# Kernel tuning notes

Measured on AMD Instinct MI355X. Metric: run time of the kernel, lower is better.

Reference implementation:

```python
import jax, jax.numpy as jnp
import numpy as np
import math

B, T, E, H = 4, 2048, 1024, 16
ALPHA = 32.0


def setup_inputs() -> dict:
    key = jax.random.key(0)
    ks = jax.random.split(key, 6)
    s = 1.0 / math.sqrt(E)
    return {
        "x": jax.random.normal(ks[0], (B, T, E), dtype=jnp.float32),
        "ch_list": 0,
        "Wq": jax.random.normal(ks[1], (E, E), dtype=jnp.float32) * s,
        "bq": jnp.zeros((E,), jnp.float32),
        "Wk": jax.random.normal(ks[2], (E, E), dtype=jnp.float32) * s,
        "bk": jnp.zeros((E,), jnp.float32),
        "Wv": jax.random.normal(ks[3], (E, E), dtype=jnp.float32) * s,
        "bv": jnp.zeros((E,), jnp.float32),
        "Wp": jax.random.normal(ks[4], (E, E), dtype=jnp.float32) * s,
        "bp": jnp.zeros((E,), jnp.float32),
    }


def reference(x, ch_list, Wq, bq, Wk, bk, Wv, bv, Wp, bp):
    Bx, Tx, Ex = x.shape
    hd = Ex // H  # head dim
    # linear projections (weights stored [in, out]); split heads -> [B,H,T,hd]
    def heads(W, b):
        return (x @ W + b).reshape(Bx, Tx, H, hd).transpose(0, 2, 1, 3)
    q, k, v = heads(Wq, bq), heads(Wk, bk), heads(Wv, bv)
    scale = 1.0 / (ALPHA * math.sqrt(hd))
    qk = jnp.einsum("bhqd,bhkd->bhqk", q * scale, k)  # [B,H,T,T]
    # extra max-rescale BEFORE the causal mask (faithful to original order)
    qk = qk - jnp.max(qk, axis=-1, keepdims=True)
    causal = jnp.tril(jnp.ones((Tx, Tx), dtype=bool))  # [T,T]
    qk = jnp.where(causal[None, None], qk, -jnp.inf)
    att = jax.nn.softmax(qk * ALPHA, axis=-1)  # dropout p=0 -> identity
    y = jnp.einsum("bhqk,bhkd->bhqd", att, v)
    y = y.transpose(0, 2, 1, 3).reshape(Bx, Tx, Ex)
    return y @ Wp + bp
```

## Files before the change

### kernel.cpp

```cpp
#include <hip/hip_runtime.h>
#include <cmath>

typedef unsigned short u16;
typedef unsigned int u32;
typedef __bf16 bf16x8 __attribute__((ext_vector_type(8)));
typedef float  floatx4 __attribute__((ext_vector_type(4)));
typedef float  floatx16 __attribute__((ext_vector_type(16)));
typedef unsigned int u32x4 __attribute__((ext_vector_type(4)));

#define T_DIM 2048
#define E_DIM 1024
#define H_DIM 16
#define HD    64
#define M_DIM 8192
#define NE    8388608
#define E2    1048576
#define QSCALE 0.18033688f

__device__ __forceinline__ u16 f2bf(float f) {
    unsigned u = __builtin_bit_cast(unsigned, f);
    return (u16)((u + 0x7FFFu + ((u >> 16) & 1u)) >> 16);
}
__device__ __forceinline__ u32 pack2bf(float f0, float f1) {
    u32 a0 = __builtin_bit_cast(u32, f0) + 0x8000u;
    u32 a1 = __builtin_bit_cast(u32, f1) + 0x8000u;
    return __builtin_amdgcn_perm(a1, a0, 0x07060302u);
}

__device__ __forceinline__ void gl_lds16(const u16* g, const u16* l) {
    __builtin_amdgcn_global_load_lds(
        (const __attribute__((address_space(1))) void*)g,
        (__attribute__((address_space(3))) void*)l,
        16, 0, 0);
}

__device__ __forceinline__ bf16x8 ld_frag(const u16* p) {
    return *(const bf16x8*)p;
}

__global__ void cvt_x_kernel(const float* __restrict__ x, u16* __restrict__ xb) {
    const size_t i = (size_t)blockIdx.x * 256 + threadIdx.x;
    const float4* s = (const float4*)x + i * 2;
    const float4 a = s[0], b = s[1];
    u16 v[8] __attribute__((aligned(16)));
    v[0]=f2bf(a.x); v[1]=f2bf(a.y); v[2]=f2bf(a.z); v[3]=f2bf(a.w);
    v[4]=f2bf(b.x); v[5]=f2bf(b.y); v[6]=f2bf(b.z); v[7]=f2bf(b.w);
    *(uint4*)(xb + i * 8) = *(const uint4*)v;
}

__global__ void transpose_cvt_kernel(const float* __restrict__ w0, const float* __restrict__ w1,
                                     const float* __restrict__ w2, const float* __restrict__ w3,
                                     u16* __restrict__ out) {
    __shared__ u16 tile[64][65];
    const float* W = blockIdx.z == 0 ? w0 : blockIdx.z == 1 ? w1 : blockIdx.z == 2 ? w2 : w3;
    u16* O = out + (size_t)blockIdx.z * E2;
    const int k0 = blockIdx.y * 64, n0 = blockIdx.x * 64;
    const int r = threadIdx.x >> 2, cp = (threadIdx.x & 3) * 16;
    const float4* src = (const float4*)&W[(size_t)(k0 + r) * E_DIM + n0 + cp];
    #pragma unroll
    for (int j4 = 0; j4 < 4; ++j4) {
        const float4 f = src[j4];
        tile[r][cp + j4*4 + 0] = f2bf(f.x);
        tile[r][cp + j4*4 + 1] = f2bf(f.y);
        tile[r][cp + j4*4 + 2] = f2bf(f.z);
        tile[r][cp + j4*4 + 3] = f2bf(f.w);
    }
    __syncthreads();
    u16 vals[16] __attribute__((aligned(16)));
    #pragma unroll
    for (int j = 0; j < 16; ++j) vals[j] = tile[cp + j][r];
    u16* dst = &O[(size_t)(n0 + r) * E_DIM + k0 + cp];
    *(uint4*)dst       = *(const uint4*)vals;
    *(uint4*)(dst + 8) = *(const uint4*)(vals + 8);
}

__global__ void transpose_v_kernel(const u16* __restrict__ v, u16* __restrict__ vt) {
    __shared__ u16 tile[64][72];
    const int bh = blockIdx.y, t0 = blockIdx.x * 64;
    const int r = threadIdx.x >> 2, cp = (threadIdx.x & 3) * 16;
    const u16* src = &v[((size_t)bh * T_DIM + t0 + r) * HD + cp];
    *(uint4*)&tile[r][cp]     = *(const uint4*)src;
    *(uint4*)&tile[r][cp + 8] = *(const uint4*)(src + 8);
    __syncthreads();
    u16 vals[16] __attribute__((aligned(16)));
    #pragma unroll
    for (int j = 0; j < 16; ++j) vals[j] = tile[cp + j][r];
    u16* dst = &vt[((size_t)bh * HD + r) * T_DIM + t0 + cp];
    *(uint4*)dst       = *(const uint4*)vals;
    *(uint4*)(dst + 8) = *(const uint4*)(vals + 8);
}

template<int REMAP>
__global__ __launch_bounds__(256)
void gemm_bf16_kernel(const u16* __restrict__ A, const u16* __restrict__ Bt,
                      const float* __restrict__ bias0, const float* __restrict__ bias1,
                      const float* __restrict__ bias2, void* __restrict__ outp)
{
    __shared__ u16 As[128 * 32];
    __shared__ u16 Bs[128 * 32];
    const int tid = threadIdx.x;
    const int w = tid >> 6, lane = tid & 63, quad = lane >> 4, l15 = lane & 15;
    const int wm = w >> 1, wn = w & 1;
    const int r0 = blockIdx.y * 128, c0 = blockIdx.x * 128;

    floatx4 acc[4][4];
    #pragma unroll
    for (int mi = 0; mi < 4; ++mi)
        #pragma unroll
        for (int ni = 0; ni < 4; ++ni)
            acc[mi][ni] = (floatx4){0.f, 0.f, 0.f, 0.f};

    for (int k0 = 0; k0 < E_DIM; k0 += 32) {
        __syncthreads();
        #pragma unroll
        for (int i = 0; i < 2; ++i) {
            const int L = i * 256 + tid;
            const unsigned off = __builtin_amdgcn_readfirstlane(i * 4096 + w * 1024);
            gl_lds16(&A [(size_t)(r0 + (L >> 2)) * E_DIM + k0 + (L & 3) * 8], (u16*)((char*)As + off));
            gl_lds16(&Bt[(size_t)(c0 + (L >> 2)) * E_DIM + k0 + (L & 3) * 8], (u16*)((char*)Bs + off));
        }
        __syncthreads();
        bf16x8 Af[4], Bf[4];
        #pragma unroll
        for (int mi = 0; mi < 4; ++mi) Af[mi] = ld_frag(&As[(wm*64 + mi*16 + l15) * 32 + quad*8]);
        #pragma unroll
        for (int ni = 0; ni < 4; ++ni) Bf[ni] = ld_frag(&Bs[(wn*64 + ni*16 + l15) * 32 + quad*8]);
        #pragma unroll
        for (int mi = 0; mi < 4; ++mi)
            #pragma unroll
            for (int ni = 0; ni < 4; ++ni)
                acc[mi][ni] = __builtin_amdgcn_mfma_f32_16x16x32_bf16(Af[mi], Bf[ni], acc[mi][ni], 0, 0, 0);
    }

    #pragma unroll
    for (int ni = 0; ni < 4; ++ni) {
        const int col = c0 + wn * 64 + ni * 16 + l15;
        float bv;
        int which = 0, cc = col;
        if (REMAP == 1) {
            which = col >> 10; cc = col & 1023;
            const float* bp_ = which == 0 ? bias0 : which == 1 ? bias1 : bias2;
            bv = bp_[cc];
        } else {
            bv = bias0[col];
        }
        #pragma unroll
        for (int mi = 0; mi < 4; ++mi) {
            #pragma unroll
            for (int r = 0; r < 4; ++r) {
                const int row = r0 + wm * 64 + mi * 16 + quad * 4 + r;
                float val = acc[mi][ni][r] + bv;
                if (REMAP == 1) {
                    if (which == 0) val *= QSCALE;
                    const int h = cc >> 6, d = cc & 63;
                    const int b = row >> 11, t = row & (T_DIM - 1);
                    ((u16*)outp)[(size_t)which * NE +
                                 (((size_t)(b * H_DIM + h) * T_DIM + t) * HD + d)] = f2bf(val);
                } else {
                    ((float*)outp)[(size_t)row * E_DIM + col] = val;
                }
            }
        }
    }
}

__global__ __launch_bounds__(256, 2)
void attn_kernel(const u16* __restrict__ q, const u16* __restrict__ k,
                 const u16* __restrict__ vt, u16* __restrict__ y)
{
    __shared__ u16 Ks[2][128 * 64];
    __shared__ u16 Vs[2][64 * 128];

    const int tid = threadIdx.x;
    const int w = tid >> 6, lane = tid & 63;
    const int hl = lane >> 5, l31 = lane & 31, l7 = lane & 7;
    const int bh = blockIdx.x;
    const int qt = gridDim.y - 1 - blockIdx.y;
    const int q0 = qt * 128;
    const int b = bh >> 4, h = bh & (H_DIM - 1);
    const size_t qkb = (size_t)bh * (T_DIM * HD);
    const size_t vtb = (size_t)bh * (HD * T_DIM);

    const int qrow = q0 + w * 32 + l31;
    bf16x8 Qf[4];
    #pragma unroll
    for (int kc = 0; kc < 4; ++kc)
        Qf[kc] = ld_frag(&q[qkb + (size_t)qrow * HD + kc * 16 + hl * 8]);

    float rsum = 0.f;
    floatx16 O[2];
    #pragma unroll
    for (int i = 0; i < 16; ++i) { O[0][i] = 0.f; O[1][i] = 0.f; }

    auto stage = [&](int jt, int sel) {
        const int j0 = jt * 128;
        #pragma unroll
        for (int i = 0; i < 4; ++i) {
            const int L = i * 256 + tid;
            const unsigned off = __builtin_amdgcn_readfirstlane(i * 4096 + w * 1024);
            {   const int row = L >> 3, ch = (L & 7) ^ (row & 7);
                gl_lds16(&k[qkb + (size_t)(j0 + row) * HD + ch * 8],
                         (u16*)((char*)&Ks[sel][0] + off)); }
            {   const int row = L >> 4, ch = (L & 15) ^ (row & 7);
                gl_lds16(&vt[vtb + (size_t)row * T_DIM + j0 + ch * 8],
                         (u16*)((char*)&Vs[sel][0] + off)); }
        }
    };

    stage(0, 0);
    for (int jt = 0; jt <= qt; ++jt) {
        __syncthreads();
        if (jt < qt) stage(jt + 1, (jt + 1) & 1);
        const u16* const Kb = &Ks[jt & 1][0];
        const u16* const Vb = &Vs[jt & 1][0];

        const bool diag = (jt == qt);
        const int nkg = diag ? (w + 1) : 4;

        #pragma unroll
        for (int kg = 0; kg < 4; ++kg) {
            if (kg < nkg) {
                floatx16 S;
                #pragma unroll
                for (int i = 0; i < 16; ++i) S[i] = 0.f;
                const int krow = kg * 32 + l31;
                #pragma unroll
                for (int kc = 0; kc < 4; ++kc) {
                    const int ch = (kc * 2 + hl) ^ l7;
                    S = __builtin_amdgcn_mfma_f32_32x32x16_bf16(
                            ld_frag(&Kb[krow * 64 + ch * 8]), Qf[kc], S, 0, 0, 0);
                }

                const bool bnd = diag && (kg == w);
                u32 u[8], ru[8];
                #pragma unroll
                for (int i = 0; i < 8; ++i) {
                    const int row0 = (2*i & 3) + 8 * (i >> 1) + 4 * hl;
                    float p0 = __builtin_amdgcn_exp2f(S[2*i]);
                    float p1 = __builtin_amdgcn_exp2f(S[2*i + 1]);
                    if (bnd && (row0     > l31)) p0 = 0.f;
                    if (bnd && (row0 + 1 > l31)) p1 = 0.f;
                    rsum += p0 + p1;
                    u[i] = pack2bf(p0, p1);
                }
                #pragma unroll
                for (int i = 0; i < 8; ++i) ru[i] = __shfl_xor(u[i], 32, 64);
                const u32x4 f0 = hl ? (u32x4){ru[2], ru[3], u[2], u[3]}
                                    : (u32x4){u[0], u[1], ru[0], ru[1]};
                const u32x4 f1 = hl ? (u32x4){ru[6], ru[7], u[6], u[7]}
                                    : (u32x4){u[4], u[5], ru[4], ru[5]};

                #pragma unroll
                for (int c2 = 0; c2 < 2; ++c2) {
                    const bf16x8 Pf = __builtin_bit_cast(bf16x8, c2 ? f1 : f0);
                    const int kc16 = kg * 4 + c2 * 2 + hl;
                    #pragma unroll
                    for (int dh = 0; dh < 2; ++dh) {
                        const int d = dh * 32 + l31;
                        const int ch = kc16 ^ l7;
                        O[dh] = __builtin_amdgcn_mfma_f32_32x32x16_bf16(
                                    Pf, ld_frag(&Vb[d * 128 + ch * 8]), O[dh], 0, 0, 0);
                    }
                }
            }
        }
    }

    rsum += __shfl_xor(rsum, 32, 64);
    const float linv = 1.0f / rsum;
    #pragma unroll
    for (int i = 0; i < 16; ++i) {
        const int qr = (i & 3) + 8 * (i >> 2) + 4 * hl;
        const float lq = __shfl(linv, qr, 32);
        const int t = q0 + w * 32 + qr;
        const size_t base = ((size_t)(b * T_DIM + t)) * E_DIM + h * HD;
        y[base + l31]      = f2bf(O[0][i] * lq);
        y[base + 32 + l31] = f2bf(O[1][i] * lq);
    }
}

extern "C" void kernel_launch(void* const* d_in, const int* in_sizes, int n_in,
                              void* d_out, int out_size, void* d_ws, size_t ws_size,
                              hipStream_t stream)
{
    const float* x  = (const float*)d_in[0];
    const float* Wq = (const float*)d_in[2];
    const float* bq = (const float*)d_in[3];
    const float* Wk = (const float*)d_in[4];
    const float* bk = (const float*)d_in[5];
    const float* Wv = (const float*)d_in[6];
    const float* bv = (const float*)d_in[7];
    const float* Wp = (const float*)d_in[8];
    const float* bp = (const float*)d_in[9];

    u16* xb  = (u16*)d_ws;
    u16* wt  = xb + NE;
    u16* qb  = wt + 4 * (size_t)E2;
    u16* kb  = qb + NE;
    u16* vb  = kb + NE;
    u16* vtb = vb + NE;
    u16* yb  = vtb + NE;

    cvt_x_kernel<<<NE / (256 * 8), 256, 0, stream>>>(x, xb);
    transpose_cvt_kernel<<<dim3(16, 16, 4), 256, 0, stream>>>(Wq, Wk, Wv, Wp, wt);
    gemm_bf16_kernel<1><<<dim3(24, 64), 256, 0, stream>>>(xb, wt, bq, bk, bv, qb);
    transpose_v_kernel<<<dim3(32, 64), 256, 0, stream>>>(vb, vtb);
    attn_kernel<<<dim3(64, 16), 256, 0, stream>>>(qb, kb, vtb, yb);
    gemm_bf16_kernel<0><<<dim3(8, 64), 256, 0, stream>>>(yb, wt + 3 * (size_t)E2, bp, bp, bp, (float*)d_out);
}
```

Measured before the change: 264.1 us.

## Fuse V transpose into QKV GEMM epilogue and swizzle GEMM LDS tiles

The QKV projection GEMM now writes the V output directly in transposed [bh, d, t] layout, packing four consecutive rows into one 8-byte store. This removes the separate transpose_v kernel and its extra read/write pass over V. The GEMM's LDS layout also gets an XOR swizzle on the 8-element k-chunks, applied on both the global-to-LDS load and the fragment reads, to cut bank conflicts. The transposed V stores are strided by T, which may be less coalesced than the old row-major writes.

New measurement: 254.4 us. 1.04x faster.

```diff
diff --git a/kernel.cpp b/kernel.cpp
--- a/kernel.cpp
+++ b/kernel.cpp
@@ -74,27 +74,12 @@
     *(uint4*)(dst + 8) = *(const uint4*)(vals + 8);
 }
 
-__global__ void transpose_v_kernel(const u16* __restrict__ v, u16* __restrict__ vt) {
-    __shared__ u16 tile[64][72];
-    const int bh = blockIdx.y, t0 = blockIdx.x * 64;
-    const int r = threadIdx.x >> 2, cp = (threadIdx.x & 3) * 16;
-    const u16* src = &v[((size_t)bh * T_DIM + t0 + r) * HD + cp];
-    *(uint4*)&tile[r][cp]     = *(const uint4*)src;
-    *(uint4*)&tile[r][cp + 8] = *(const uint4*)(src + 8);
-    __syncthreads();
-    u16 vals[16] __attribute__((aligned(16)));
-    #pragma unroll
-    for (int j = 0; j < 16; ++j) vals[j] = tile[cp + j][r];
-    u16* dst = &vt[((size_t)bh * HD + r) * T_DIM + t0 + cp];
-    *(uint4*)dst       = *(const uint4*)vals;
-    *(uint4*)(dst + 8) = *(const uint4*)(vals + 8);
-}
-
 template<int REMAP>
 __global__ __launch_bounds__(256)
 void gemm_bf16_kernel(const u16* __restrict__ A, const u16* __restrict__ Bt,
                       const float* __restrict__ bias0, const float* __restrict__ bias1,
-                      const float* __restrict__ bias2, void* __restrict__ outp)
+                      const float* __restrict__ bias2, void* __restrict__ outp,
+                      u16* __restrict__ vtp)
 {
     __shared__ u16 As[128 * 32];
     __shared__ u16 Bs[128 * 32];
@@ -110,21 +95,25 @@
         for (int ni = 0; ni < 4; ++ni)
             acc[mi][ni] = (floatx4){0.f, 0.f, 0.f, 0.f};
 
+    const int fsw = (quad ^ ((l15 >> 1) & 3)) * 8;
+
     for (int k0 = 0; k0 < E_DIM; k0 += 32) {
         __syncthreads();
         #pragma unroll
         for (int i = 0; i < 2; ++i) {
             const int L = i * 256 + tid;
+            const int row = L >> 2, s = L & 3;
+            const int c = s ^ ((row >> 1) & 3);
             const unsigned off = __builtin_amdgcn_readfirstlane(i * 4096 + w * 1024);
-            gl_lds16(&A [(size_t)(r0 + (L >> 2)) * E_DIM + k0 + (L & 3) * 8], (u16*)((char*)As + off));
-            gl_lds16(&Bt[(size_t)(c0 + (L >> 2)) * E_DIM + k0 + (L & 3) * 8], (u16*)((char*)Bs + off));
+            gl_lds16(&A [(size_t)(r0 + row) * E_DIM + k0 + c * 8], (u16*)((char*)As + off));
+            gl_lds16(&Bt[(size_t)(c0 + row) * E_DIM + k0 + c * 8], (u16*)((char*)Bs + off));
         }
         __syncthreads();
         bf16x8 Af[4], Bf[4];
         #pragma unroll
-        for (int mi = 0; mi < 4; ++mi) Af[mi] = ld_frag(&As[(wm*64 + mi*16 + l15) * 32 + quad*8]);
-        #pragma unroll
-        for (int ni = 0; ni < 4; ++ni) Bf[ni] = ld_frag(&Bs[(wn*64 + ni*16 + l15) * 32 + quad*8]);
+        for (int mi = 0; mi < 4; ++mi) Af[mi] = ld_frag(&As[(wm*64 + mi*16 + l15) * 32 + fsw]);
+        #pragma unroll
+        for (int ni = 0; ni < 4; ++ni) Bf[ni] = ld_frag(&Bs[(wn*64 + ni*16 + l15) * 32 + fsw]);
         #pragma unroll
         for (int mi = 0; mi < 4; ++mi)
             #pragma unroll
@@ -146,18 +135,28 @@
         }
         #pragma unroll
         for (int mi = 0; mi < 4; ++mi) {
-            #pragma unroll
-            for (int r = 0; r < 4; ++r) {
-                const int row = r0 + wm * 64 + mi * 16 + quad * 4 + r;
-                float val = acc[mi][ni][r] + bv;
-                if (REMAP == 1) {
-                    if (which == 0) val *= QSCALE;
-                    const int h = cc >> 6, d = cc & 63;
-                    const int b = row >> 11, t = row & (T_DIM - 1);
-                    ((u16*)outp)[(size_t)which * NE +
-                                 (((size_t)(b * H_DIM + h) * T_DIM + t) * HD + d)] = f2bf(val);
-                } else {
-                    ((float*)outp)[(size_t)row * E_DIM + col] = val;
+            if (REMAP == 1 && which == 2) {
+                const int h = cc >> 6, d = cc & 63;
+                const int row0 = r0 + wm * 64 + mi * 16 + quad * 4;
+                const int b = row0 >> 11, t0 = row0 & (T_DIM - 1);
+                uint2 pk;
+                pk.x = pack2bf(acc[mi][ni][0] + bv, acc[mi][ni][1] + bv);
+                pk.y = pack2bf(acc[mi][ni][2] + bv, acc[mi][ni][3] + bv);
+                *(uint2*)&vtp[((size_t)((b * H_DIM + h) * HD + d)) * T_DIM + t0] = pk;
+            } else {
+                #pragma unroll
+                for (int r = 0; r < 4; ++r) {
+                    const int row = r0 + wm * 64 + mi * 16 + quad * 4 + r;
+                    float val = acc[mi][ni][r] + bv;
+                    if (REMAP == 1) {
+                        if (which == 0) val *= QSCALE;
+                        const int h = cc >> 6, d = cc & 63;
+                        const int b = row >> 11, t = row & (T_DIM - 1);
+                        ((u16*)outp)[(size_t)which * NE +
+                                     (((size_t)(b * H_DIM + h) * T_DIM + t) * HD + d)] = f2bf(val);
+                    } else {
+                        ((float*)outp)[(size_t)row * E_DIM + col] = val;
+                    }
                 }
             }
         }
@@ -297,14 +296,12 @@
     u16* wt  = xb + NE;
     u16* qb  = wt + 4 * (size_t)E2;
     u16* kb  = qb + NE;
-    u16* vb  = kb + NE;
-    u16* vtb = vb + NE;
+    u16* vtb = kb + NE;
     u16* yb  = vtb + NE;
 
     cvt_x_kernel<<<NE / (256 * 8), 256, 0, stream>>>(x, xb);
     transpose_cvt_kernel<<<dim3(16, 16, 4), 256, 0, stream>>>(Wq, Wk, Wv, Wp, wt);
-    gemm_bf16_kernel<1><<<dim3(24, 64), 256, 0, stream>>>(xb, wt, bq, bk, bv, qb);
-    transpose_v_kernel<<<dim3(32, 64), 256, 0, stream>>>(vb, vtb);
+    gemm_bf16_kernel<1><<<dim3(24, 64), 256, 0, stream>>>(xb, wt, bq, bk, bv, qb, vtb);
     attn_kernel<<<dim3(64, 16), 256, 0, stream>>>(qb, kb, vtb, yb);
-    gemm_bf16_kernel<0><<<dim3(8, 64), 256, 0, stream>>>(yb, wt + 3 * (size_t)E2, bp, bp, bp, (float*)d_out);
-}
+    gemm_bf16_kernel<0><<<dim3(8, 64), 256, 0, stream>>>(yb, wt + 3 * (size_t)E2, bp, bp, bp, (float*)d_out, nullptr);
+}
```
